# Performance work log

Hardware: AMD Instinct MI355X
Metric: run time of the kernel (lower is better)

## Reference

```python
import jax, jax.numpy as jnp
import numpy as np

N = 100000
E = 3200000
D = 128
EPS = 1e-12  # F.normalize default eps


def setup_inputs() -> dict:
    key = jax.random.key(0)
    ks = jax.random.split(key, 8)
    inp = {
        "edge_index": jax.random.randint(ks[0], (2, E), 0, N, dtype=jnp.int64)
        if jax.config.jax_enable_x64 else jax.random.randint(ks[0], (2, E), 0, N, dtype=jnp.int32),
        "emb_weight": jax.random.normal(ks[1], (N, D), dtype=jnp.float32) / np.sqrt(D),
        "lin_l_w0": jax.random.normal(ks[2], (D, D), dtype=jnp.float32) / np.sqrt(D),
        "lin_l_b0": jax.random.normal(ks[3], (D,), dtype=jnp.float32) * 0.01,
        "lin_r_w0": jax.random.normal(ks[4], (D, D), dtype=jnp.float32) / np.sqrt(D),
        "lin_l_w1": jax.random.normal(ks[5], (D, D), dtype=jnp.float32) / np.sqrt(D),
        "lin_l_b1": jax.random.normal(ks[6], (D,), dtype=jnp.float32) * 0.01,
        "lin_r_w1": jax.random.normal(ks[7], (D, D), dtype=jnp.float32) / np.sqrt(D),
    }
    return inp


def _sage_conv(x, src, dst, deg_inv, lin_l_w, lin_l_b, lin_r_w):
    # mean aggregation of source features at destination nodes
    agg = jax.ops.segment_sum(x[src], dst, num_segments=N) * deg_inv  # [N, D]
    # out = lin_l(agg) + lin_r(x); torch Linear: y = x @ W.T + b
    return agg @ lin_l_w.T + lin_l_b + x @ lin_r_w.T


def reference(edge_index, emb_weight, lin_l_w0, lin_l_b0, lin_r_w0,
              lin_l_w1, lin_l_b1, lin_r_w1):
    src, dst = edge_index[0], edge_index[1]
    deg = jax.ops.segment_sum(jnp.ones((E,), jnp.float32), dst, num_segments=N)
    deg_inv = jnp.where(deg > 0, 1.0 / jnp.maximum(deg, 1.0), 0.0)[:, None]  # [N,1]

    x = emb_weight
    x = _sage_conv(x, src, dst, deg_inv, lin_l_w0, lin_l_b0, lin_r_w0)
    x = jax.nn.relu(x)
    x = _sage_conv(x, src, dst, deg_inv, lin_l_w1, lin_l_b1, lin_r_w1)
    # F.normalize(x, p=2, dim=1): x / max(||x||_2, eps)
    norm = jnp.linalg.norm(x, axis=1, keepdims=True)
    return x / jnp.maximum(norm, EPS)
```

## Files before the change

kernel.cpp:

```cpp
#include <hip/hip_runtime.h>

typedef unsigned int uint;
typedef unsigned short ushort;
typedef __bf16 v8b __attribute__((ext_vector_type(8)));
typedef float v4f __attribute__((ext_vector_type(4)));

#define NN 100000
#define EE 3200000
#define DD 128

#define BSH 8
#define BSZ 256
#define NB ((NN + BSZ - 1) / BSZ)
#define CAP 16384
#define EPB 8192
#define NBLK1 ((EE + EPB - 1) / EPB)

#define LGRID ((NN + 127) / 128)

#define PB_B0 NBLK1
#define PB_EMBB 12500
#define PB_B1 (PB_B0 + PB_EMBB)
#define PB_WB 64
#define PB_B2 (PB_B1 + PB_WB)
#define PB_GRID (PB_B2 + 1)

__device__ __attribute__((aligned(256))) int g_offs[NN + 1];
__device__ __attribute__((aligned(256))) int g_bcnt2[NB];
__device__ __attribute__((aligned(256))) int g_bbase[NB];
__device__ __attribute__((aligned(256))) int g_csr[EE];
__device__ __attribute__((aligned(256))) uint g_pairs2[(size_t)NB * CAP];
__device__ __attribute__((aligned(256))) ushort g_emb_h[(size_t)NN * DD];
__device__ __attribute__((aligned(256))) ushort g_emb_l[(size_t)NN * DD];
__device__ __attribute__((aligned(256))) ushort g_agg_h[(size_t)NN * DD];
__device__ __attribute__((aligned(256))) ushort g_agg_l[(size_t)NN * DD];
__device__ __attribute__((aligned(256))) ushort g_hh[(size_t)NN * DD];
__device__ __attribute__((aligned(256))) ushort g_hl[(size_t)NN * DD];
__device__ __attribute__((aligned(256))) ushort g_w_h[4][DD * DD];
__device__ __attribute__((aligned(256))) ushort g_w_l[4][DD * DD];
__device__ __attribute__((aligned(256))) float g_biasf[2][DD];

__device__ __forceinline__ float blo(uint u) { return __uint_as_float(u << 16); }
__device__ __forceinline__ float bhi(uint u) { return __uint_as_float(u & 0xffff0000u); }
__device__ __forceinline__ ushort f2b(float f) {
  uint u = __float_as_uint(f);
  u += 0x7fffu + ((u >> 16) & 1u);
  return (ushort)(u >> 16);
}
__device__ __forceinline__ float b2f(ushort s) { return __uint_as_float(((uint)s) << 16); }

__device__ __forceinline__ int ld_src(const int* __restrict__ ei, int is64, int e) {
  int v = is64 ? ei[2 * e] : ei[e];
  return ((uint)v < (uint)NN) ? v : 0;
}
__device__ __forceinline__ int ld_dst(const int* __restrict__ ei, int is64, int e) {
  int v = is64 ? ei[2 * (EE + e)] : ei[EE + e];
  return ((uint)v < (uint)NN) ? v : 0;
}

__device__ __forceinline__ void split4f(const void* __restrict__ src,
                                        ushort* __restrict__ dh,
                                        ushort* __restrict__ dl, int i, int isf32) {
  float f[4];
  if (isf32) {
    float4 v = *(const float4*)((const float*)src + i);
    f[0] = v.x; f[1] = v.y; f[2] = v.z; f[3] = v.w;
  } else {
    ushort4 s = *(const ushort4*)((const ushort*)src + i);
    f[0] = b2f(s.x); f[1] = b2f(s.y); f[2] = b2f(s.z); f[3] = b2f(s.w);
  }
  ushort4 h, l;
  ushort* hp = &h.x;
  ushort* lp = &l.x;
#pragma unroll
  for (int k = 0; k < 4; k++) {
    ushort hi = f2b(f[k]);
    hp[k] = hi;
    lp[k] = f2b(f[k] - b2f(hi));
  }
  *(ushort4*)(dh + i) = h;
  *(ushort4*)(dl + i) = l;
}

__global__ __launch_bounds__(256) void k_pb(
    const int* __restrict__ ei, const void* __restrict__ emb,
    const void* __restrict__ s0, const void* __restrict__ s1,
    const void* __restrict__ s2, const void* __restrict__ s3,
    const void* __restrict__ bs0, const void* __restrict__ bs1) {
  __shared__ int s_cnt[NB];
  __shared__ int s_base[NB];
  __shared__ int s_flag;
  int bid = blockIdx.x;
  int tid = threadIdx.x;
  if (bid < PB_B0) {
    if (tid == 0) s_flag = 0;
    for (int i = tid; i < NB; i += 256) s_cnt[i] = 0;
    __syncthreads();
    int base = bid * EPB;
    int v = 0;
#pragma unroll
    for (int k = 0; k < 8; k++) {
      int e = base + k * 256 + tid;
      if (e < EE) v |= ei[2 * e + 1];
    }
    if (v) atomicOr(&s_flag, 1);
    __syncthreads();
    int is64 = (s_flag == 0) ? 1 : 0;
    uint pk[32];
    uint bb[16];
#pragma unroll
    for (int k = 0; k < 32; k++) {
      int e = base + k * 256 + tid;
      uint b = 0xffffu;
      uint p = 0;
      if (e < EE) {
        int d = ld_dst(ei, is64, e);
        int s = ld_src(ei, is64, e);
        b = (uint)(d >> BSH);
        p = ((uint)(d & (BSZ - 1)) << 17) | (uint)s;
        atomicAdd(&s_cnt[(int)b], 1);
      }
      pk[k] = p;
      if ((k & 1) == 0) bb[k >> 1] = b;
      else bb[k >> 1] |= b << 16;
    }
    __syncthreads();
    for (int i = tid; i < NB; i += 256) {
      int c = s_cnt[i];
      s_base[i] = c ? atomicAdd(&g_bcnt2[i], c) : 0;
      s_cnt[i] = 0;
    }
    __syncthreads();
#pragma unroll
    for (int k = 0; k < 32; k++) {
      uint b = (bb[k >> 1] >> ((k & 1) * 16)) & 0xffffu;
      if (b != 0xffffu) {
        int idx = s_base[b] + atomicAdd(&s_cnt[b], 1);
        if (idx < CAP) g_pairs2[(size_t)b * CAP + idx] = pk[k];
      }
    }
  } else {
    if (tid == 0) s_flag = 0;
    __syncthreads();
    const ushort* u = (const ushort*)emb;
    int bad = 0;
    for (int i = tid; i < 2048; i += 256) {
      int e = (u[2 * i] >> 7) & 0xff;
      if (e < 0x40 || e > 0x7f) bad = 1;
    }
    if (bad) atomicOr(&s_flag, 1);
    __syncthreads();
    int isf32 = s_flag;
    if (bid < PB_B1) {
      int i = ((bid - PB_B0) * 256 + tid) * 4;
      split4f(emb, g_emb_h, g_emb_l, i, isf32);
    } else if (bid < PB_B2) {
      int wb = bid - PB_B1;
      int w = wb >> 4;
      int i = ((wb & 15) * 256 + tid) * 4;
      const void* src = (w == 0) ? s0 : (w == 1) ? s1 : (w == 2) ? s2 : s3;
      split4f(src, &g_w_h[0][0] + w * DD * DD, &g_w_l[0][0] + w * DD * DD, i, isf32);
    } else {
      int which = tid >> 7;
      int i = tid & 127;
      const void* src = which ? bs1 : bs0;
      float vv = isf32 ? ((const float*)src)[i] : b2f(((const ushort*)src)[i]);
      g_biasf[which][i] = vv;
    }
  }
}

__global__ void k_bscan() {
  __shared__ int sd[512];
  int t = threadIdx.x;
  int v = (t < NB) ? min(g_bcnt2[t], CAP) : 0;
  sd[t] = v;
  __syncthreads();
  for (int off = 1; off < 512; off <<= 1) {
    int x = (t >= off) ? sd[t - off] : 0;
    __syncthreads();
    sd[t] += x;
    __syncthreads();
  }
  if (t < NB) g_bbase[t] = sd[t] - v;
  if (t == 511) g_offs[NN] = sd[511];
}

__global__ __launch_bounds__(256) void k_place() {
  int b = blockIdx.x;
  int n = min(g_bcnt2[b], CAP);
  int gbase = g_bbase[b];
  const uint* pr = g_pairs2 + (size_t)b * CAP;
  __shared__ int hist[BSZ];
  __shared__ int sd[BSZ];
  __shared__ int cur[BSZ];
  int t = threadIdx.x;
  hist[t] = 0;
  __syncthreads();
  for (int e = t; e < n; e += 256) atomicAdd(&hist[pr[e] >> 17], 1);
  __syncthreads();
  int v = hist[t];
  sd[t] = v;
  __syncthreads();
  for (int off = 1; off < BSZ; off <<= 1) {
    int x = (t >= off) ? sd[t - off] : 0;
    __syncthreads();
    sd[t] += x;
    __syncthreads();
  }
  int excl = sd[t] - v;
  int node = (b << BSH) + t;
  if (node < NN) g_offs[node] = gbase + excl;
  cur[t] = excl;
  __syncthreads();
  for (int e = t; e < n; e += 256) {
    uint pk = pr[e];
    int p = atomicAdd(&cur[pk >> 17], 1);
    g_csr[gbase + p] = (int)(pk & 0x1FFFFu);
  }
  __syncthreads();
  if (t == 0) g_bcnt2[b] = 0;
}

__global__ void k_agg(const ushort* __restrict__ x) {
  int lane = threadIdx.x & 63;
  int node = (blockIdx.x * blockDim.x + threadIdx.x) >> 6;
  int beg = g_offs[node], end = g_offs[node + 1];
  int eb = lane >> 4;
  int col = (lane & 15) * 8;
  float a[8];
#pragma unroll
  for (int i = 0; i < 8; i++) a[i] = 0.f;
  for (int c = beg; c < end; c += 64) {
    int cnt = end - c;
    if (cnt > 64) cnt = 64;
    int my = g_csr[c + (lane < cnt ? lane : cnt - 1)];
    if ((uint)my >= (uint)NN) my = 0;
    int j = 0;
    for (; j + 16 <= cnt; j += 16) {
      int s0 = __shfl(my, j + eb);
      int s1 = __shfl(my, j + 4 + eb);
      int s2 = __shfl(my, j + 8 + eb);
      int s3 = __shfl(my, j + 12 + eb);
      uint4 r0 = *(const uint4*)(x + (size_t)s0 * DD + col);
      uint4 r1 = *(const uint4*)(x + (size_t)s1 * DD + col);
      uint4 r2 = *(const uint4*)(x + (size_t)s2 * DD + col);
      uint4 r3 = *(const uint4*)(x + (size_t)s3 * DD + col);
      a[0] += blo(r0.x); a[1] += bhi(r0.x); a[2] += blo(r0.y); a[3] += bhi(r0.y);
      a[4] += blo(r0.z); a[5] += bhi(r0.z); a[6] += blo(r0.w); a[7] += bhi(r0.w);
      a[0] += blo(r1.x); a[1] += bhi(r1.x); a[2] += blo(r1.y); a[3] += bhi(r1.y);
      a[4] += blo(r1.z); a[5] += bhi(r1.z); a[6] += blo(r1.w); a[7] += bhi(r1.w);
      a[0] += blo(r2.x); a[1] += bhi(r2.x); a[2] += blo(r2.y); a[3] += bhi(r2.y);
      a[4] += blo(r2.z); a[5] += bhi(r2.z); a[6] += blo(r2.w); a[7] += bhi(r2.w);
      a[0] += blo(r3.x); a[1] += bhi(r3.x); a[2] += blo(r3.y); a[3] += bhi(r3.y);
      a[4] += blo(r3.z); a[5] += bhi(r3.z); a[6] += blo(r3.w); a[7] += bhi(r3.w);
    }
    for (; j + 8 <= cnt; j += 8) {
      int s0 = __shfl(my, j + eb);
      int s1 = __shfl(my, j + 4 + eb);
      uint4 r0 = *(const uint4*)(x + (size_t)s0 * DD + col);
      uint4 r1 = *(const uint4*)(x + (size_t)s1 * DD + col);
      a[0] += blo(r0.x); a[1] += bhi(r0.x); a[2] += blo(r0.y); a[3] += bhi(r0.y);
      a[4] += blo(r0.z); a[5] += bhi(r0.z); a[6] += blo(r0.w); a[7] += bhi(r0.w);
      a[0] += blo(r1.x); a[1] += bhi(r1.x); a[2] += blo(r1.y); a[3] += bhi(r1.y);
      a[4] += blo(r1.z); a[5] += bhi(r1.z); a[6] += blo(r1.w); a[7] += bhi(r1.w);
    }
    for (; j < cnt; j += 4) {
      int e = j + eb;
      int s = __shfl(my, e < cnt ? e : 0);
      float w = e < cnt ? 1.f : 0.f;
      uint4 r = *(const uint4*)(x + (size_t)s * DD + col);
      a[0] = fmaf(blo(r.x), w, a[0]); a[1] = fmaf(bhi(r.x), w, a[1]);
      a[2] = fmaf(blo(r.y), w, a[2]); a[3] = fmaf(bhi(r.y), w, a[3]);
      a[4] = fmaf(blo(r.z), w, a[4]); a[5] = fmaf(bhi(r.z), w, a[5]);
      a[6] = fmaf(blo(r.w), w, a[6]); a[7] = fmaf(bhi(r.w), w, a[7]);
    }
  }
#pragma unroll
  for (int i = 0; i < 8; i++) {
    a[i] += __shfl_xor(a[i], 16);
    a[i] += __shfl_xor(a[i], 32);
  }
  int deg = end - beg;
  float inv = deg > 0 ? 1.0f / (float)deg : 0.f;
  if (lane < 16) {
    uint4 h, l;
    uint* hp = &h.x;
    uint* lp = &l.x;
#pragma unroll
    for (int k = 0; k < 4; k++) {
      float f0 = a[2 * k] * inv, f1 = a[2 * k + 1] * inv;
      ushort h0 = f2b(f0), h1 = f2b(f1);
      ushort l0 = f2b(f0 - b2f(h0)), l1 = f2b(f1 - b2f(h1));
      hp[k] = (uint)h0 | ((uint)h1 << 16);
      lp[k] = (uint)l0 | ((uint)l1 << 16);
    }
    size_t o = (size_t)node * DD + col;
    *(uint4*)(g_agg_h + o) = h;
    *(uint4*)(g_agg_l + o) = l;
  }
}


#define MFMA16(a, b, c) __builtin_amdgcn_mfma_f32_16x16x32_bf16(a, b, c, 0, 0, 0)

template <int MODE>
__global__ __launch_bounds__(256, 2) void k_lin(
    const ushort* __restrict__ A1h, const ushort* __restrict__ A1l,
    const ushort* __restrict__ A2h, const ushort* __restrict__ A2l,
    const ushort* __restrict__ Wlh, const ushort* __restrict__ Wll,
    const ushort* __restrict__ Wrh, const ushort* __restrict__ Wrl,
    const float* __restrict__ bias, void* out0, ushort* __restrict__ outlo) {
  __shared__ ushort smem[16384];
  int tid = threadIdx.x;
  int lane = tid & 63;
  int wid = tid >> 6;
  int m = lane & 15, q = lane >> 4;
  int row0 = blockIdx.x * 128 + wid * 32;
  int arow0 = row0 + m;      if (arow0 > NN - 1) arow0 = NN - 1;
  int arow1 = row0 + 16 + m; if (arow1 > NN - 1) arow1 = NN - 1;
  size_t aoff0 = (size_t)arow0 * DD + q * 8;
  size_t aoff1 = (size_t)arow1 * DD + q * 8;
  v8b a1h[2][4], a1l[2][4], a2h[2][4], a2l[2][4];
#pragma unroll
  for (int ks = 0; ks < 4; ks++) {
    a1h[0][ks] = *(const v8b*)(A1h + aoff0 + ks * 32);
    a1l[0][ks] = *(const v8b*)(A1l + aoff0 + ks * 32);
    a2h[0][ks] = *(const v8b*)(A2h + aoff0 + ks * 32);
    a2l[0][ks] = *(const v8b*)(A2l + aoff0 + ks * 32);
    a1h[1][ks] = *(const v8b*)(A1h + aoff1 + ks * 32);
    a1l[1][ks] = *(const v8b*)(A1l + aoff1 + ks * 32);
    a2h[1][ks] = *(const v8b*)(A2h + aoff1 + ks * 32);
    a2l[1][ks] = *(const v8b*)(A2l + aoff1 + ks * 32);
  }
  v4f acc[2][8];
#pragma unroll
  for (int t = 0; t < 2; t++)
#pragma unroll
    for (int nt = 0; nt < 8; nt++) acc[t][nt] = (v4f){0.f, 0.f, 0.f, 0.f};
#pragma unroll
  for (int st = 0; st < 4; st++) {
#pragma unroll
    for (int k = 0; k < 8; k++) {
      int arr = k >> 1;
      int n = ((k & 1) << 4) + (tid >> 4);
      int cb16 = tid & 15;
      const ushort* srcp = (arr == 0) ? Wlh : (arr == 1) ? Wll : (arr == 2) ? Wrh : Wrl;
      uint4 v = *(const uint4*)(srcp + (size_t)(st * 32 + n) * DD + cb16 * 8);
      *(uint4*)(smem + arr * 4096 + n * 128 + ((cb16 ^ (n & 15)) << 3)) = v;
    }
    __syncthreads();
#pragma unroll
    for (int ks = 0; ks < 4; ks++) {
#pragma unroll
      for (int ntl = 0; ntl < 2; ntl++) {
        int nt = st * 2 + ntl;
        int nl = ntl * 16 + m;
        int u = nl * 128 + (((q + 4 * ks) ^ m) << 3);
        v8b blh = *(const v8b*)(smem + u);
        v8b bll = *(const v8b*)(smem + 4096 + u);
        v8b brh = *(const v8b*)(smem + 8192 + u);
        v8b brl = *(const v8b*)(smem + 12288 + u);
        acc[0][nt] = MFMA16(a1h[0][ks], blh, acc[0][nt]);
        acc[0][nt] = MFMA16(a1h[0][ks], bll, acc[0][nt]);
        acc[0][nt] = MFMA16(a1l[0][ks], blh, acc[0][nt]);
        acc[0][nt] = MFMA16(a2h[0][ks], brh, acc[0][nt]);
        acc[0][nt] = MFMA16(a2h[0][ks], brl, acc[0][nt]);
        acc[0][nt] = MFMA16(a2l[0][ks], brh, acc[0][nt]);
        acc[1][nt] = MFMA16(a1h[1][ks], blh, acc[1][nt]);
        acc[1][nt] = MFMA16(a1h[1][ks], bll, acc[1][nt]);
        acc[1][nt] = MFMA16(a1l[1][ks], blh, acc[1][nt]);
        acc[1][nt] = MFMA16(a2h[1][ks], brh, acc[1][nt]);
        acc[1][nt] = MFMA16(a2h[1][ks], brl, acc[1][nt]);
        acc[1][nt] = MFMA16(a2l[1][ks], brh, acc[1][nt]);
      }
    }
    __syncthreads();
  }
  if (MODE == 0) {
    ushort* oh = (ushort*)out0;
#pragma unroll
    for (int t = 0; t < 2; t++) {
#pragma unroll
      for (int nt = 0; nt < 8; nt++) {
        float bv = bias[nt * 16 + m];
#pragma unroll
        for (int r = 0; r < 4; r++) {
          int row = row0 + t * 16 + q * 4 + r;
          if (row < NN) {
            float v = acc[t][nt][r] + bv;
            v = v > 0.f ? v : 0.f;
            ushort hi = f2b(v);
            ushort lo = f2b(v - b2f(hi));
            size_t o = (size_t)row * DD + nt * 16 + m;
            oh[o] = hi;
            outlo[o] = lo;
          }
        }
      }
    }
  } else {
    float* of = (float*)out0;
#pragma unroll
    for (int t = 0; t < 2; t++) {
#pragma unroll
      for (int r = 0; r < 4; r++) {
        float p = 0.f;
#pragma unroll
        for (int nt = 0; nt < 8; nt++) {
          float v = acc[t][nt][r] + bias[nt * 16 + m];
          acc[t][nt][r] = v;
          p += v * v;
        }
        p += __shfl_xor(p, 1);
        p += __shfl_xor(p, 2);
        p += __shfl_xor(p, 4);
        p += __shfl_xor(p, 8);
        float inv = (p > 0.f) ? 1.0f / fmaxf(sqrtf(p), 1e-12f) : 0.f;
        int row = row0 + t * 16 + q * 4 + r;
        if (row < NN) {
#pragma unroll
          for (int nt = 0; nt < 8; nt++)
            of[(size_t)row * DD + nt * 16 + m] = acc[t][nt][r] * inv;
        }
      }
    }
  }
}


extern "C" void kernel_launch(void* const* d_in, const int* in_sizes, int n_in,
                              void* d_out, int out_size, void* d_ws, size_t ws_size,
                              hipStream_t stream) {
  const int* ei = (const int*)d_in[0];
  (void)in_sizes; (void)n_in; (void)out_size; (void)d_ws; (void)ws_size;

  ushort* wh;  hipGetSymbolAddress((void**)&wh, HIP_SYMBOL(g_w_h));
  ushort* wl;  hipGetSymbolAddress((void**)&wl, HIP_SYMBOL(g_w_l));
  ushort* wl0h = wh, *wr0h = wh + DD * DD, *wl1h = wh + 2 * DD * DD, *wr1h = wh + 3 * DD * DD;
  ushort* wl0l = wl, *wr0l = wl + DD * DD, *wl1l = wl + 2 * DD * DD, *wr1l = wl + 3 * DD * DD;
  float* bf;   hipGetSymbolAddress((void**)&bf, HIP_SYMBOL(g_biasf));
  float* b0 = bf, *b1 = bf + DD;
  ushort* eh;  hipGetSymbolAddress((void**)&eh, HIP_SYMBOL(g_emb_h));
  ushort* el;  hipGetSymbolAddress((void**)&el, HIP_SYMBOL(g_emb_l));
  ushort* ah;  hipGetSymbolAddress((void**)&ah, HIP_SYMBOL(g_agg_h));
  ushort* al;  hipGetSymbolAddress((void**)&al, HIP_SYMBOL(g_agg_l));
  ushort* hh;  hipGetSymbolAddress((void**)&hh, HIP_SYMBOL(g_hh));
  ushort* hl;  hipGetSymbolAddress((void**)&hl, HIP_SYMBOL(g_hl));

  k_pb<<<PB_GRID, 256, 0, stream>>>(ei, d_in[1], d_in[2], d_in[4], d_in[5],
                                    d_in[7], d_in[3], d_in[6]);
  k_bscan<<<1, 512, 0, stream>>>();
  k_place<<<NB, 256, 0, stream>>>();

  k_agg<<<NN / 4, 256, 0, stream>>>(eh);
  k_lin<0><<<LGRID, 256, 0, stream>>>(ah, al, eh, el, wl0h, wl0l, wr0h, wr0l, b0, hh, hl);
  k_agg<<<NN / 4, 256, 0, stream>>>(hh);
  k_lin<1><<<LGRID, 256, 0, stream>>>(ah, al, hh, hl, wl1h, wl1l, wr1h, wr1l, b1, d_out, nullptr);
}
```

Baseline: 495.1 us.

## Stage bucketed edge pairs in LDS for coalesced scatter; use nontemporal loads/stores

The edge bucketing kernel now computes a block-local prefix sum over bucket histograms, sorts the packed pairs into shared memory by bucket, then writes them to global memory in contiguous runs instead of scattering each pair separately. This is meant to cut uncoalesced global writes. Separately, the aggregation kernel reads CSR indices and writes its outputs with nontemporal hints to reduce cache pollution. The change adds about 50KB of LDS per block and several extra barriers from the scan, which lowers occupancy in the bucketing kernel.

```diff
diff --git a/kernel.cpp b/kernel.cpp
--- a/kernel.cpp
+++ b/kernel.cpp
@@ -4,6 +4,7 @@
 typedef unsigned short ushort;
 typedef __bf16 v8b __attribute__((ext_vector_type(8)));
 typedef float v4f __attribute__((ext_vector_type(4)));
+typedef uint v4u __attribute__((ext_vector_type(4)));
 
 #define NN 100000
 #define EE 3200000
@@ -87,14 +88,18 @@
     const void* __restrict__ s0, const void* __restrict__ s1,
     const void* __restrict__ s2, const void* __restrict__ s3,
     const void* __restrict__ bs0, const void* __restrict__ bs1) {
-  __shared__ int s_cnt[NB];
+  __shared__ uint s_spk[EPB];
+  __shared__ ushort s_sbk[EPB];
+  __shared__ int s_hist[NB];
+  __shared__ int s_loff[NB + 1];
   __shared__ int s_base[NB];
+  __shared__ int s_part[256];
   __shared__ int s_flag;
   int bid = blockIdx.x;
   int tid = threadIdx.x;
   if (bid < PB_B0) {
     if (tid == 0) s_flag = 0;
-    for (int i = tid; i < NB; i += 256) s_cnt[i] = 0;
+    for (int i = tid; i < NB; i += 256) s_hist[i] = 0;
     __syncthreads();
     int base = bid * EPB;
     int v = 0;
@@ -118,26 +123,50 @@
         int s = ld_src(ei, is64, e);
         b = (uint)(d >> BSH);
         p = ((uint)(d & (BSZ - 1)) << 17) | (uint)s;
-        atomicAdd(&s_cnt[(int)b], 1);
+        atomicAdd(&s_hist[(int)b], 1);
       }
       pk[k] = p;
       if ((k & 1) == 0) bb[k >> 1] = b;
       else bb[k >> 1] |= b << 16;
     }
     __syncthreads();
+    int c0 = (2 * tid < NB) ? s_hist[2 * tid] : 0;
+    int c1 = (2 * tid + 1 < NB) ? s_hist[2 * tid + 1] : 0;
+    s_part[tid] = c0 + c1;
+    __syncthreads();
+    for (int off = 1; off < 256; off <<= 1) {
+      int x = (tid >= off) ? s_part[tid - off] : 0;
+      __syncthreads();
+      s_part[tid] += x;
+      __syncthreads();
+    }
+    int excl = s_part[tid] - (c0 + c1);
+    if (2 * tid < NB) s_loff[2 * tid] = excl;
+    if (2 * tid + 1 < NB) s_loff[2 * tid + 1] = excl + c0;
+    if (tid == 255) s_loff[NB] = s_part[255];
+    __syncthreads();
     for (int i = tid; i < NB; i += 256) {
-      int c = s_cnt[i];
+      int c = s_loff[i + 1] - s_loff[i];
       s_base[i] = c ? atomicAdd(&g_bcnt2[i], c) : 0;
-      s_cnt[i] = 0;
+      s_hist[i] = 0;
     }
     __syncthreads();
 #pragma unroll
     for (int k = 0; k < 32; k++) {
       uint b = (bb[k >> 1] >> ((k & 1) * 16)) & 0xffffu;
       if (b != 0xffffu) {
-        int idx = s_base[b] + atomicAdd(&s_cnt[b], 1);
-        if (idx < CAP) g_pairs2[(size_t)b * CAP + idx] = pk[k];
+        int slot = s_loff[b] + atomicAdd(&s_hist[b], 1);
+        s_spk[slot] = pk[k];
+        s_sbk[slot] = (ushort)b;
       }
+    }
+    __syncthreads();
+    int tot = s_loff[NB];
+    for (int slot = tid; slot < tot; slot += 256) {
+      int b = s_sbk[slot];
+      int gaddr = s_base[b] + (slot - s_loff[b]);
+      if (gaddr < CAP)
+        __builtin_nontemporal_store(s_spk[slot], &g_pairs2[(size_t)b * CAP + gaddr]);
     }
   } else {
     if (tid == 0) s_flag = 0;
@@ -234,7 +263,7 @@
   for (int c = beg; c < end; c += 64) {
     int cnt = end - c;
     if (cnt > 64) cnt = 64;
-    int my = g_csr[c + (lane < cnt ? lane : cnt - 1)];
+    int my = __builtin_nontemporal_load(&g_csr[c + (lane < cnt ? lane : cnt - 1)]);
     if ((uint)my >= (uint)NN) my = 0;
     int j = 0;
     for (; j + 16 <= cnt; j += 16) {
@@ -284,20 +313,18 @@
   int deg = end - beg;
   float inv = deg > 0 ? 1.0f / (float)deg : 0.f;
   if (lane < 16) {
-    uint4 h, l;
-    uint* hp = &h.x;
-    uint* lp = &l.x;
+    v4u h, l;
 #pragma unroll
     for (int k = 0; k < 4; k++) {
       float f0 = a[2 * k] * inv, f1 = a[2 * k + 1] * inv;
       ushort h0 = f2b(f0), h1 = f2b(f1);
       ushort l0 = f2b(f0 - b2f(h0)), l1 = f2b(f1 - b2f(h1));
-      hp[k] = (uint)h0 | ((uint)h1 << 16);
-      lp[k] = (uint)l0 | ((uint)l1 << 16);
+      h[k] = (uint)h0 | ((uint)h1 << 16);
+      l[k] = (uint)l0 | ((uint)l1 << 16);
     }
     size_t o = (size_t)node * DD + col;
-    *(uint4*)(g_agg_h + o) = h;
-    *(uint4*)(g_agg_l + o) = l;
+    __builtin_nontemporal_store(h, (v4u*)(g_agg_h + o));
+    __builtin_nontemporal_store(l, (v4u*)(g_agg_l + o));
   }
 }
 
```

Result: slower. 539.9 us (+9.0%).
